# Performance work log

Hardware: AMD Instinct MI355X
Metric: run time of the kernel (lower is better)

## Reference

```python
import jax, jax.numpy as jnp
import numpy as np

N_NODES = 50000
N_EDGES = 800000
D = 128

def setup_inputs() -> dict:
    key = jax.random.key(0)
    ks = jax.random.split(key, 10)
    return {
        "nf": jax.random.normal(ks[0], (N_NODES, D), jnp.float32),
        "ef": jax.random.normal(ks[1], (N_EDGES, D), jnp.float32),
        "W_node": jax.random.normal(ks[2], (D, D), jnp.float32) * (1.0 / np.sqrt(D)),
        "W_edge": jax.random.normal(ks[3], (D, D), jnp.float32) * (1.0 / np.sqrt(D)),
        "node_bias": jax.random.normal(ks[4], (D,), jnp.float32) * 0.01,
        "edge_bias": jax.random.normal(ks[5], (D,), jnp.float32) * 0.01,
        "dense_W": jax.random.normal(ks[6], (2 * D, D), jnp.float32) * (1.0 / np.sqrt(2 * D)),
        "dense_b": jax.random.normal(ks[7], (D,), jnp.float32) * 0.01,
        "src": jax.random.randint(ks[8], (N_EDGES,), 0, N_NODES, jnp.int32),
        "dst": jax.random.randint(ks[9], (N_EDGES,), 0, N_NODES, jnp.int32),
    }

def reference(nf, ef, W_node, W_edge, node_bias, edge_bias, dense_W, dense_b, src, dst):
    N = nf.shape[0]
    # linear projections (dropout p=0 -> identity)
    nf1 = nf @ W_node                       # [N, D]
    ef1 = ef @ W_edge                       # [E, D]
    # update_all: mean of incoming edge features per destination node
    s = jax.ops.segment_sum(ef1, dst, num_segments=N)                       # [N, D]
    deg = jax.ops.segment_sum(jnp.ones_like(ef1[:, 0]), dst, num_segments=N)  # [N]
    nb_ef = s / jnp.maximum(deg, 1.0)[:, None]  # zero for isolated nodes
    # apply_nodes: bias + activation on nf (nb_ef unchanged)
    nf2 = jax.nn.relu(nf1 + node_bias)          # [N, D]
    # apply_edges: gather-concat-dense update with bias + activation
    tmp_ef = ef1 + nb_ef[dst]                   # [E, D]
    srcdst_nf = (nf2[src] + nf2[dst]) * 0.5     # [E, D]
    ef2 = jnp.concatenate([tmp_ef, srcdst_nf], axis=1) @ dense_W + dense_b + edge_bias
    ef2 = jax.nn.relu(ef2)                      # [E, D]
    return nf2, ef2
```

## Files before the change

### kernel.cpp

```cpp
#include <hip/hip_runtime.h>

#define D 128

__device__ __forceinline__ float4 f4zero() { return make_float4(0.f, 0.f, 0.f, 0.f); }

#define FMA4(accv, s, wv) \
    (accv).x += (s) * (wv).x; (accv).y += (s) * (wv).y; \
    (accv).z += (s) * (wv).z; (accv).w += (s) * (wv).w;

template <int MODE>
__global__ __launch_bounds__(256) void gemm128(
    const float* __restrict__ A, const float* __restrict__ W,
    const float* __restrict__ bias, float* __restrict__ C, int M,
    const int* __restrict__ dst, float* __restrict__ sG, float* __restrict__ deg)
{
    __shared__ float Wl[128 * 128];
    __shared__ float At[128 * 64];

    const int tid = threadIdx.x;
    const int row0 = blockIdx.x * 64;

    {
        const float4* W4 = (const float4*)W;
        float4* Wl4 = (float4*)Wl;
#pragma unroll
        for (int i = 0; i < 16; ++i) Wl4[tid + i * 256] = W4[tid + i * 256];
    }
    {
        const int r = tid & 63;
        const int row = row0 + r;
        const bool ok = (row < M);
        const float4* Arow = (const float4*)(A + (size_t)row * D);
#pragma unroll
        for (int kg = tid >> 6; kg < 32; kg += 4) {
            float4 v = ok ? Arow[kg] : f4zero();
            At[(kg * 4 + 0) * 64 + r] = v.x;
            At[(kg * 4 + 1) * 64 + r] = v.y;
            At[(kg * 4 + 2) * 64 + r] = v.z;
            At[(kg * 4 + 3) * 64 + r] = v.w;
        }
    }
    __syncthreads();

    const int tc = tid & 15;
    const int tr = tid >> 4;

    float4 acc[4][2];
#pragma unroll
    for (int i = 0; i < 4; ++i) { acc[i][0] = f4zero(); acc[i][1] = f4zero(); }

#pragma unroll 2
    for (int k = 0; k < 128; ++k) {
        const float4 a  = *(const float4*)&At[k * 64 + 4 * tr];
        const float4 w0 = *(const float4*)&Wl[k * 128 + 4 * tc];
        const float4 w1 = *(const float4*)&Wl[k * 128 + 64 + 4 * tc];
        FMA4(acc[0][0], a.x, w0); FMA4(acc[0][1], a.x, w1);
        FMA4(acc[1][0], a.y, w0); FMA4(acc[1][1], a.y, w1);
        FMA4(acc[2][0], a.z, w0); FMA4(acc[2][1], a.z, w1);
        FMA4(acc[3][0], a.w, w0); FMA4(acc[3][1], a.w, w1);
    }

    float4 b0 = f4zero(), b1 = f4zero();
    if (MODE == 0) {
        b0 = ((const float4*)bias)[tc];
        b1 = ((const float4*)bias)[16 + tc];
    }

#pragma unroll
    for (int i = 0; i < 4; ++i) {
        const int row = row0 + 4 * tr + i;
        if (row >= M) continue;
        float4 v0 = acc[i][0], v1 = acc[i][1];
        if (MODE == 0) {
            v0.x = fmaxf(v0.x + b0.x, 0.f); v0.y = fmaxf(v0.y + b0.y, 0.f);
            v0.z = fmaxf(v0.z + b0.z, 0.f); v0.w = fmaxf(v0.w + b0.w, 0.f);
            v1.x = fmaxf(v1.x + b1.x, 0.f); v1.y = fmaxf(v1.y + b1.y, 0.f);
            v1.z = fmaxf(v1.z + b1.z, 0.f); v1.w = fmaxf(v1.w + b1.w, 0.f);
        }
        if (MODE == 1) {
            v0.x *= 0.5f; v0.y *= 0.5f; v0.z *= 0.5f; v0.w *= 0.5f;
            v1.x *= 0.5f; v1.y *= 0.5f; v1.z *= 0.5f; v1.w *= 0.5f;
        }
        float4* Crow = (float4*)(C + (size_t)row * D);
        Crow[tc] = v0;
        Crow[16 + tc] = v1;
        if (MODE == 2) {
            const int d = dst[row];
            float* srow = sG + (size_t)d * D;
            atomicAdd(&srow[4 * tc + 0], v0.x);
            atomicAdd(&srow[4 * tc + 1], v0.y);
            atomicAdd(&srow[4 * tc + 2], v0.z);
            atomicAdd(&srow[4 * tc + 3], v0.w);
            atomicAdd(&srow[64 + 4 * tc + 0], v1.x);
            atomicAdd(&srow[64 + 4 * tc + 1], v1.y);
            atomicAdd(&srow[64 + 4 * tc + 2], v1.z);
            atomicAdd(&srow[64 + 4 * tc + 3], v1.w);
            if (tc == 0) atomicAdd(&deg[d], 1.0f);
        }
    }
}

__global__ __launch_bounds__(256) void wcombo_k(
    const float* __restrict__ We, const float* __restrict__ dW, float* __restrict__ out)
{
    const int i = blockIdx.x * 2 + (threadIdx.x >> 7);
    const int j = threadIdx.x & 127;
    float acc = 0.f;
#pragma unroll 4
    for (int k = 0; k < 128; ++k) acc += We[i * 128 + k] * dW[k * 128 + j];
    out[i * 128 + j] = acc;
}

__global__ __launch_bounds__(256) void edge_final(
    float* __restrict__ G, const float* __restrict__ sG, const float* __restrict__ deg,
    const float* __restrict__ Q, const int* __restrict__ src, const int* __restrict__ dst,
    const float* __restrict__ dense_b, const float* __restrict__ edge_bias, int E)
{
    const int e = blockIdx.x * 8 + (threadIdx.x >> 5);
    const int c = threadIdx.x & 31;
    if (e >= E) return;
    const int d = dst[e];
    const int s = src[e];
    const float r = 1.0f / fmaxf(deg[d], 1.0f);

    float4* Grow = (float4*)(G + (size_t)e * D);
    const float4 g  = Grow[c];
    const float4 sg = ((const float4*)(sG + (size_t)d * D))[c];
    const float4 qs = ((const float4*)(Q + (size_t)s * D))[c];
    const float4 qd = ((const float4*)(Q + (size_t)d * D))[c];
    const float4 b  = ((const float4*)dense_b)[c];
    const float4 eb = ((const float4*)edge_bias)[c];

    float4 o;
    o.x = fmaxf(g.x + sg.x * r + qs.x + qd.x + b.x + eb.x, 0.f);
    o.y = fmaxf(g.y + sg.y * r + qs.y + qd.y + b.y + eb.y, 0.f);
    o.z = fmaxf(g.z + sg.z * r + qs.z + qd.z + b.z + eb.z, 0.f);
    o.w = fmaxf(g.w + sg.w * r + qs.w + qd.w + b.w + eb.w, 0.f);
    Grow[c] = o;
}

extern "C" void kernel_launch(void* const* d_in, const int* in_sizes, int n_in,
                              void* d_out, int out_size, void* d_ws, size_t ws_size,
                              hipStream_t stream)
{
    const float* nf        = (const float*)d_in[0];
    const float* ef        = (const float*)d_in[1];
    const float* W_node    = (const float*)d_in[2];
    const float* W_edge    = (const float*)d_in[3];
    const float* node_bias = (const float*)d_in[4];
    const float* edge_bias = (const float*)d_in[5];
    const float* dense_W   = (const float*)d_in[6];
    const float* dense_b   = (const float*)d_in[7];
    const int*   src       = (const int*)d_in[8];
    const int*   dst       = (const int*)d_in[9];

    const int N = in_sizes[0] / D;
    const int E = in_sizes[1] / D;

    float* out_nf2 = (float*)d_out;
    float* G       = (float*)d_out + (size_t)N * D;

    float* ws     = (float*)d_ws;
    float* wcombo = ws;
    float* Q      = wcombo + 128 * 128;
    float* sG     = Q + (size_t)N * D;
    float* deg    = sG + (size_t)N * D;

    hipMemsetAsync(sG, 0, (size_t)N * D * sizeof(float), stream);
    hipMemsetAsync(deg, 0, (size_t)N * sizeof(float), stream);

    wcombo_k<<<64, 256, 0, stream>>>(W_edge, dense_W, wcombo);

    gemm128<0><<<(N + 63) / 64, 256, 0, stream>>>(
        nf, W_node, node_bias, out_nf2, N, nullptr, nullptr, nullptr);
    gemm128<1><<<(N + 63) / 64, 256, 0, stream>>>(
        out_nf2, dense_W + 128 * 128, nullptr, Q, N, nullptr, nullptr, nullptr);
    gemm128<2><<<(E + 63) / 64, 256, 0, stream>>>(
        ef, wcombo, nullptr, G, E, dst, sG, deg);
    edge_final<<<(E + 7) / 8, 256, 0, stream>>>(
        G, sG, deg, Q, src, dst, dense_b, edge_bias, E);
}
```

Measured before the change: 2.570 ms.

## Replace atomic scatter with CSR segment mean and fuse edge epilogue into GEMM

Builds a CSR by destination (histogram, scan, scatter), takes the per-node mean of raw edge features, and projects that mean through the combined weight. Because the projection is linear, this gives the mean of projected features at node granularity, and the edge GEMM epilogue then gathers it and fuses the final bias, gather and ReLU. This removes 100M float atomics and the separate edge_final pass over the output. The GEMM is restructured so each thread holds two rows by 32 columns and reads A directly from global memory, with 512-thread blocks. The costs are an irregular gather over ef in segsum, a single-block serial scan, and a different floating-point summation order.

```diff
diff --git a/kernel.cpp b/kernel.cpp
--- a/kernel.cpp
+++ b/kernel.cpp
@@ -5,97 +5,116 @@
 __device__ __forceinline__ float4 f4zero() { return make_float4(0.f, 0.f, 0.f, 0.f); }
 
 #define FMA4(accv, s, wv) \
-    (accv).x += (s) * (wv).x; (accv).y += (s) * (wv).y; \
-    (accv).z += (s) * (wv).z; (accv).w += (s) * (wv).w;
+    (accv).x = fmaf((s), (wv).x, (accv).x); (accv).y = fmaf((s), (wv).y, (accv).y); \
+    (accv).z = fmaf((s), (wv).z, (accv).z); (accv).w = fmaf((s), (wv).w, (accv).w);
+
+#define ADD4(o, a, b) \
+    (o).x = (a).x + (b).x; (o).y = (a).y + (b).y; (o).z = (a).z + (b).z; (o).w = (a).w + (b).w;
+
+#define M_NODE 0
+#define M_HALF 1
+#define M_RQ   2
+#define M_EDGE 3
 
 template <int MODE>
-__global__ __launch_bounds__(256) void gemm128(
-    const float* __restrict__ A, const float* __restrict__ W,
-    const float* __restrict__ bias, float* __restrict__ C, int M,
-    const int* __restrict__ dst, float* __restrict__ sG, float* __restrict__ deg)
-{
-    __shared__ float Wl[128 * 128];
-    __shared__ float At[128 * 64];
-
+__global__ __launch_bounds__(512, 4) void gemm_v(
+    const float* __restrict__ A, const float* __restrict__ W, float* __restrict__ C, int M,
+    const float* __restrict__ bias,
+    const float* __restrict__ R, const float* __restrict__ Q,
+    const int* __restrict__ src, const int* __restrict__ dst,
+    const float* __restrict__ b1, const float* __restrict__ b2)
+{
+    __shared__ float Wl[D * D];
     const int tid = threadIdx.x;
-    const int row0 = blockIdx.x * 64;
-
     {
         const float4* W4 = (const float4*)W;
         float4* Wl4 = (float4*)Wl;
 #pragma unroll
-        for (int i = 0; i < 16; ++i) Wl4[tid + i * 256] = W4[tid + i * 256];
-    }
-    {
-        const int r = tid & 63;
-        const int row = row0 + r;
-        const bool ok = (row < M);
-        const float4* Arow = (const float4*)(A + (size_t)row * D);
-#pragma unroll
-        for (int kg = tid >> 6; kg < 32; kg += 4) {
-            float4 v = ok ? Arow[kg] : f4zero();
-            At[(kg * 4 + 0) * 64 + r] = v.x;
-            At[(kg * 4 + 1) * 64 + r] = v.y;
-            At[(kg * 4 + 2) * 64 + r] = v.z;
-            At[(kg * 4 + 3) * 64 + r] = v.w;
-        }
-    }
-    __syncthreads();
-
-    const int tc = tid & 15;
-    const int tr = tid >> 4;
-
-    float4 acc[4][2];
-#pragma unroll
-    for (int i = 0; i < 4; ++i) { acc[i][0] = f4zero(); acc[i][1] = f4zero(); }
+        for (int i = 0; i < 8; ++i) Wl4[tid + i * 512] = W4[tid + i * 512];
+    }
+    __syncthreads();
+
+    const int lane = tid & 63;
+    const int wv = tid >> 6;
+    const int rowWave = wv >> 2;
+    const int colBase = (wv & 3) * 32;
+
+    const int r0 = blockIdx.x * 256 + rowWave * 128 + lane;
+    const int r1 = r0 + 64;
+    const bool ok0 = (r0 < M), ok1 = (r1 < M);
+    const float* A0 = A + (size_t)(ok0 ? r0 : 0) * D;
+    const float* A1 = A + (size_t)(ok1 ? r1 : 0) * D;
+
+    float4 acc0[8], acc1[8];
+#pragma unroll
+    for (int j = 0; j < 8; ++j) { acc0[j] = f4zero(); acc1[j] = f4zero(); }
 
 #pragma unroll 2
-    for (int k = 0; k < 128; ++k) {
-        const float4 a  = *(const float4*)&At[k * 64 + 4 * tr];
-        const float4 w0 = *(const float4*)&Wl[k * 128 + 4 * tc];
-        const float4 w1 = *(const float4*)&Wl[k * 128 + 64 + 4 * tc];
-        FMA4(acc[0][0], a.x, w0); FMA4(acc[0][1], a.x, w1);
-        FMA4(acc[1][0], a.y, w0); FMA4(acc[1][1], a.y, w1);
-        FMA4(acc[2][0], a.z, w0); FMA4(acc[2][1], a.z, w1);
-        FMA4(acc[3][0], a.w, w0); FMA4(acc[3][1], a.w, w1);
-    }
-
-    float4 b0 = f4zero(), b1 = f4zero();
-    if (MODE == 0) {
-        b0 = ((const float4*)bias)[tc];
-        b1 = ((const float4*)bias)[16 + tc];
-    }
-
-#pragma unroll
-    for (int i = 0; i < 4; ++i) {
-        const int row = row0 + 4 * tr + i;
-        if (row >= M) continue;
-        float4 v0 = acc[i][0], v1 = acc[i][1];
-        if (MODE == 0) {
-            v0.x = fmaxf(v0.x + b0.x, 0.f); v0.y = fmaxf(v0.y + b0.y, 0.f);
-            v0.z = fmaxf(v0.z + b0.z, 0.f); v0.w = fmaxf(v0.w + b0.w, 0.f);
-            v1.x = fmaxf(v1.x + b1.x, 0.f); v1.y = fmaxf(v1.y + b1.y, 0.f);
-            v1.z = fmaxf(v1.z + b1.z, 0.f); v1.w = fmaxf(v1.w + b1.w, 0.f);
-        }
-        if (MODE == 1) {
-            v0.x *= 0.5f; v0.y *= 0.5f; v0.z *= 0.5f; v0.w *= 0.5f;
-            v1.x *= 0.5f; v1.y *= 0.5f; v1.z *= 0.5f; v1.w *= 0.5f;
-        }
-        float4* Crow = (float4*)(C + (size_t)row * D);
-        Crow[tc] = v0;
-        Crow[16 + tc] = v1;
-        if (MODE == 2) {
+    for (int k = 0; k < D; k += 4) {
+        const float4 a0 = *(const float4*)(A0 + k);
+        const float4 a1 = *(const float4*)(A1 + k);
+#pragma unroll
+        for (int kk = 0; kk < 4; ++kk) {
+            const float av0 = (&a0.x)[kk];
+            const float av1 = (&a1.x)[kk];
+            const float* wrow = &Wl[(k + kk) * D + colBase];
+#pragma unroll
+            for (int j = 0; j < 8; ++j) {
+                const float4 w = *(const float4*)(wrow + 4 * j);
+                FMA4(acc0[j], av0, w);
+                FMA4(acc1[j], av1, w);
+            }
+        }
+    }
+
+    __syncthreads();
+
+#pragma unroll
+    for (int rr = 0; rr < 2; ++rr) {
+        const int row = rr ? r1 : r0;
+        if (!(rr ? ok1 : ok0)) continue;
+        float4* accp = rr ? acc1 : acc0;
+        float4* Crow = (float4*)(C + (size_t)row * D + colBase);
+        if (MODE == M_NODE) {
+            const float4* B = (const float4*)bias + (colBase >> 2);
+#pragma unroll
+            for (int j = 0; j < 8; ++j) {
+                float4 v; ADD4(v, accp[j], B[j]);
+                v.x = fmaxf(v.x, 0.f); v.y = fmaxf(v.y, 0.f);
+                v.z = fmaxf(v.z, 0.f); v.w = fmaxf(v.w, 0.f);
+                Crow[j] = v;
+            }
+        } else if (MODE == M_HALF) {
+#pragma unroll
+            for (int j = 0; j < 8; ++j) {
+                float4 v = accp[j];
+                v.x *= 0.5f; v.y *= 0.5f; v.z *= 0.5f; v.w *= 0.5f;
+                Crow[j] = v;
+            }
+        } else if (MODE == M_RQ) {
+            const float4* Qr = (const float4*)(Q + (size_t)row * D + colBase);
+            const float4* B1 = (const float4*)b1 + (colBase >> 2);
+            const float4* B2 = (const float4*)b2 + (colBase >> 2);
+#pragma unroll
+            for (int j = 0; j < 8; ++j) {
+                float4 v; ADD4(v, accp[j], Qr[j]);
+                float4 bb; ADD4(bb, B1[j], B2[j]);
+                ADD4(v, v, bb);
+                Crow[j] = v;
+            }
+        } else {
             const int d = dst[row];
-            float* srow = sG + (size_t)d * D;
-            atomicAdd(&srow[4 * tc + 0], v0.x);
-            atomicAdd(&srow[4 * tc + 1], v0.y);
-            atomicAdd(&srow[4 * tc + 2], v0.z);
-            atomicAdd(&srow[4 * tc + 3], v0.w);
-            atomicAdd(&srow[64 + 4 * tc + 0], v1.x);
-            atomicAdd(&srow[64 + 4 * tc + 1], v1.y);
-            atomicAdd(&srow[64 + 4 * tc + 2], v1.z);
-            atomicAdd(&srow[64 + 4 * tc + 3], v1.w);
-            if (tc == 0) atomicAdd(&deg[d], 1.0f);
+            const int s = src[row];
+            const float4* RQr = (const float4*)(R + (size_t)d * D + colBase);
+            const float4* Qs  = (const float4*)(Q + (size_t)s * D + colBase);
+#pragma unroll
+            for (int j = 0; j < 8; ++j) {
+                float4 v; ADD4(v, accp[j], RQr[j]);
+                ADD4(v, v, Qs[j]);
+                v.x = fmaxf(v.x, 0.f); v.y = fmaxf(v.y, 0.f);
+                v.z = fmaxf(v.z, 0.f); v.w = fmaxf(v.w, 0.f);
+                Crow[j] = v;
+            }
         }
     }
 }
@@ -107,36 +126,96 @@
     const int j = threadIdx.x & 127;
     float acc = 0.f;
 #pragma unroll 4
-    for (int k = 0; k < 128; ++k) acc += We[i * 128 + k] * dW[k * 128 + j];
-    out[i * 128 + j] = acc;
-}
-
-__global__ __launch_bounds__(256) void edge_final(
-    float* __restrict__ G, const float* __restrict__ sG, const float* __restrict__ deg,
-    const float* __restrict__ Q, const int* __restrict__ src, const int* __restrict__ dst,
-    const float* __restrict__ dense_b, const float* __restrict__ edge_bias, int E)
-{
-    const int e = blockIdx.x * 8 + (threadIdx.x >> 5);
+    for (int k = 0; k < D; ++k) acc = fmaf(We[i * D + k], dW[k * D + j], acc);
+    out[i * D + j] = acc;
+}
+
+__global__ __launch_bounds__(256) void hist_k(const int* __restrict__ dst,
+                                              int* __restrict__ cnt, int E)
+{
+    const int e = blockIdx.x * 256 + threadIdx.x;
+    if (e < E) atomicAdd(&cnt[dst[e]], 1);
+}
+
+__global__ __launch_bounds__(1024) void scan_k(const int* __restrict__ cnt,
+                                               int* __restrict__ rowptr,
+                                               int* __restrict__ cursor, int N, int E)
+{
+    __shared__ int wsum[16];
+    __shared__ int woff[16];
+    __shared__ int tot_s;
+    __shared__ int carry_s;
+    const int tid = threadIdx.x, lane = tid & 63, wv = tid >> 6;
+    if (tid == 0) carry_s = 0;
+    __syncthreads();
+    for (int base = 0; base < N; base += 1024) {
+        const int i = base + tid;
+        const int v = (i < N) ? cnt[i] : 0;
+        int x = v;
+#pragma unroll
+        for (int off = 1; off < 64; off <<= 1) {
+            int t = __shfl_up(x, off);
+            if (lane >= off) x += t;
+        }
+        if (lane == 63) wsum[wv] = x;
+        __syncthreads();
+        if (wv == 0) {
+            int s = (lane < 16) ? wsum[lane] : 0;
+#pragma unroll
+            for (int off = 1; off < 16; off <<= 1) {
+                int t = __shfl_up(s, off);
+                if (lane >= off) s += t;
+            }
+            if (lane < 16) woff[lane] = s - wsum[lane];
+            if (lane == 15) tot_s = s;
+        }
+        __syncthreads();
+        const int excl = x - v + woff[wv] + carry_s;
+        if (i < N) { rowptr[i] = excl; cursor[i] = excl; }
+        __syncthreads();
+        if (tid == 0) carry_s += tot_s;
+        __syncthreads();
+    }
+    if (tid == 0) rowptr[N] = E;
+}
+
+__global__ __launch_bounds__(256) void scatter_k(const int* __restrict__ dst,
+                                                 int* __restrict__ cursor,
+                                                 int* __restrict__ eidx, int E)
+{
+    const int e = blockIdx.x * 256 + threadIdx.x;
+    if (e < E) {
+        const int p = atomicAdd(&cursor[dst[e]], 1);
+        eidx[p] = e;
+    }
+}
+
+__global__ __launch_bounds__(256) void segsum_k(const float* __restrict__ ef,
+                                                const int* __restrict__ rowptr,
+                                                const int* __restrict__ eidx,
+                                                float* __restrict__ Sn)
+{
+    const int n = blockIdx.x;
+    const int start = rowptr[n], end = rowptr[n + 1];
     const int c = threadIdx.x & 31;
-    if (e >= E) return;
-    const int d = dst[e];
-    const int s = src[e];
-    const float r = 1.0f / fmaxf(deg[d], 1.0f);
-
-    float4* Grow = (float4*)(G + (size_t)e * D);
-    const float4 g  = Grow[c];
-    const float4 sg = ((const float4*)(sG + (size_t)d * D))[c];
-    const float4 qs = ((const float4*)(Q + (size_t)s * D))[c];
-    const float4 qd = ((const float4*)(Q + (size_t)d * D))[c];
-    const float4 b  = ((const float4*)dense_b)[c];
-    const float4 eb = ((const float4*)edge_bias)[c];
-
-    float4 o;
-    o.x = fmaxf(g.x + sg.x * r + qs.x + qd.x + b.x + eb.x, 0.f);
-    o.y = fmaxf(g.y + sg.y * r + qs.y + qd.y + b.y + eb.y, 0.f);
-    o.z = fmaxf(g.z + sg.z * r + qs.z + qd.z + b.z + eb.z, 0.f);
-    o.w = fmaxf(g.w + sg.w * r + qs.w + qd.w + b.w + eb.w, 0.f);
-    Grow[c] = o;
+    const int slot = threadIdx.x >> 5;
+    float4 acc = f4zero();
+    for (int i = start + slot; i < end; i += 8) {
+        const int e = eidx[i];
+        const float4 v = ((const float4*)ef)[(size_t)e * 32 + c];
+        ADD4(acc, acc, v);
+    }
+    __shared__ float4 red[8][32];
+    red[slot][c] = acc;
+    __syncthreads();
+    if (slot == 0) {
+        float4 s = red[0][c];
+#pragma unroll
+        for (int r = 1; r < 8; ++r) { ADD4(s, s, red[r][c]); }
+        const float inv = 1.0f / fmaxf((float)(end - start), 1.0f);
+        s.x *= inv; s.y *= inv; s.z *= inv; s.w *= inv;
+        ((float4*)Sn)[(size_t)n * 32 + c] = s;
+    }
 }
 
 extern "C" void kernel_launch(void* const* d_in, const int* in_sizes, int n_in,
@@ -158,25 +237,34 @@
     const int E = in_sizes[1] / D;
 
     float* out_nf2 = (float*)d_out;
-    float* G       = (float*)d_out + (size_t)N * D;
-
-    float* ws     = (float*)d_ws;
-    float* wcombo = ws;
-    float* Q      = wcombo + 128 * 128;
-    float* sG     = Q + (size_t)N * D;
-    float* deg    = sG + (size_t)N * D;
-
-    hipMemsetAsync(sG, 0, (size_t)N * D * sizeof(float), stream);
-    hipMemsetAsync(deg, 0, (size_t)N * sizeof(float), stream);
+    float* out_ef2 = (float*)d_out + (size_t)N * D;
+
+    float* wcombo = (float*)d_ws;
+    float* Q      = wcombo + D * D;
+    float* SnRQ   = Q + (size_t)N * D;
+    int*   cnt    = (int*)(SnRQ + (size_t)N * D);
+    int*   rowptr = cnt + N;
+    int*   cursor = rowptr + N + 1;
+    int*   eidx   = cursor + N;
+
+    hipMemsetAsync(cnt, 0, (size_t)N * sizeof(int), stream);
 
     wcombo_k<<<64, 256, 0, stream>>>(W_edge, dense_W, wcombo);
 
-    gemm128<0><<<(N + 63) / 64, 256, 0, stream>>>(
-        nf, W_node, node_bias, out_nf2, N, nullptr, nullptr, nullptr);
-    gemm128<1><<<(N + 63) / 64, 256, 0, stream>>>(
-        out_nf2, dense_W + 128 * 128, nullptr, Q, N, nullptr, nullptr, nullptr);
-    gemm128<2><<<(E + 63) / 64, 256, 0, stream>>>(
-        ef, wcombo, nullptr, G, E, dst, sG, deg);
-    edge_final<<<(E + 7) / 8, 256, 0, stream>>>(
-        G, sG, deg, Q, src, dst, dense_b, edge_bias, E);
-}
+    gemm_v<M_NODE><<<(N + 255) / 256, 512, 0, stream>>>(
+        nf, W_node, out_nf2, N, node_bias, nullptr, nullptr, nullptr, nullptr, nullptr, nullptr);
+    gemm_v<M_HALF><<<(N + 255) / 256, 512, 0, stream>>>(
+        out_nf2, dense_W + D * D, Q, N, nullptr, nullptr, nullptr, nullptr, nullptr, nullptr, nullptr);
+
+    hist_k<<<(E + 255) / 256, 256, 0, stream>>>(dst, cnt, E);
+    scan_k<<<1, 1024, 0, stream>>>(cnt, rowptr, cursor, N, E);
+    scatter_k<<<(E + 255) / 256, 256, 0, stream>>>(dst, cursor, eidx, E);
+
+    segsum_k<<<N, 256, 0, stream>>>(ef, rowptr, eidx, SnRQ);
+
+    gemm_v<M_RQ><<<(N + 255) / 256, 512, 0, stream>>>(
+        SnRQ, wcombo, SnRQ, N, nullptr, nullptr, Q, nullptr, nullptr, dense_b, edge_bias);
+
+    gemm_v<M_EDGE><<<(E + 255) / 256, 512, 0, stream>>>(
+        ef, wcombo, out_ef2, E, nullptr, SnRQ, Q, src, dst, nullptr, nullptr);
+}
```

Measured after the change: 2.190 ms. 14.8% less time.
